# Optimization experiments

Hardware: AMD Instinct MI355X
Metric: run time of the kernel (lower is better)

The kernel has to match this reference:

```python
import jax, jax.numpy as jnp
import numpy as np

N_NODES = 50000
N_EDGES = 800000
N_GRAPHS = 50
N_OBS = 4
N_FEAT = 64
N_LAYERS = 3


def setup_inputs() -> dict:
    key = jax.random.key(0)
    ks = jax.random.split(key, 12)
    x = jax.random.normal(ks[0], (N_NODES, N_OBS), dtype=jnp.float32)
    # every node appears at least once as a target (col) so degree > 0 everywhere
    row = jax.random.randint(ks[1], (N_EDGES,), 0, N_NODES, dtype=jnp.int32)
    col = jnp.concatenate([
        jnp.arange(N_NODES, dtype=jnp.int32),
        jax.random.randint(ks[2], (N_EDGES - N_NODES,), 0, N_NODES, dtype=jnp.int32),
    ])
    edge_index = jnp.stack([row, col])  # [2, E]
    batch = jnp.repeat(jnp.arange(N_GRAPHS, dtype=jnp.int32), N_NODES // N_GRAPHS)

    def w(k, shape):
        fan_in = shape[0]
        return jax.random.normal(k, shape, dtype=jnp.float32) / jnp.sqrt(jnp.float32(fan_in))

    return {
        "x": x,
        "W_init": w(ks[3], (N_OBS, N_FEAT)),
        "W_e1": w(ks[4], (N_OBS, N_FEAT - 1)),
        "W_e2": w(ks[5], (N_FEAT, N_FEAT)),
        "W_msg": w(ks[6], (N_LAYERS, 2 * N_FEAT, N_FEAT)),
        "W_upd": w(ks[7], (N_LAYERS, 2 * N_FEAT, N_FEAT)),
        "W_pool": w(ks[8], (N_FEAT, N_FEAT)),
        "W_read": w(ks[9], (2 * N_FEAT, 1)),
        "b_read": jnp.zeros((1,), dtype=jnp.float32),
        "edge_index": edge_index,
        "batch": batch,
        "batch_size": N_GRAPHS,
    }


def reference(x, W_init, W_e1, W_e2, W_msg, W_upd, W_pool, W_read, b_read,
              edge_index, batch, batch_size):
    n = x.shape[0]
    row, col = edge_index[0], edge_index[1]
    # in-degree at target nodes (PyG degree(col, N))
    deg = jax.ops.segment_sum(jnp.ones_like(col, dtype=x.dtype), col, num_segments=n)
    deg_inv = (1.0 / deg)[:, None]  # [N,1]

    # node init embedding
    cur = jax.nn.relu(x @ W_init)  # [N,F]

    # EdgeAndNodeEmbeddingLayer
    h = jax.nn.relu(x @ W_e1)  # [N,F-1]
    agg = deg_inv * jax.ops.segment_sum(h[row], col, num_segments=n)  # [N,F-1]
    y = jnp.concatenate([agg, (deg / deg.max())[:, None]], axis=1)  # [N,F]
    edge_emb = jax.nn.relu(y @ W_e2)  # [N,F]

    # UpdateNodeEmbeddingLayer x n_layers
    for i in range(W_msg.shape[0]):
        nagg = deg_inv * jax.ops.segment_sum(cur[row], col, num_segments=n)
        msg = jax.nn.relu(jnp.concatenate([nagg, edge_emb], axis=-1) @ W_msg[i])
        cur = jax.nn.relu(jnp.concatenate([cur, msg], axis=-1) @ W_upd[i])

    # ReadoutLayer (graphs are equal-sized, batch is sorted -> means[batch])
    counts = jax.ops.segment_sum(jnp.ones((n,), dtype=x.dtype), batch, num_segments=batch_size)
    means = jax.ops.segment_sum(cur, batch, num_segments=batch_size) / counts[:, None]
    global_pool = means[batch]  # [N,F]
    f_pooled = global_pool @ W_pool
    features = jax.nn.relu(jnp.concatenate([f_pooled, cur], axis=-1))  # [N,2F]
    out = features @ W_read + b_read  # [N,1]
    return out
```

## Files before the change

### kernel.cpp

```cpp
#include <hip/hip_runtime.h>
#include <hip/hip_bf16.h>

#define N_NODES 50000
#define N_EDGES 800000
#define NF      64
#define NG      50
#define NPG     (N_NODES / NG)
#define SCAN_NBLK ((N_NODES + 255) / 256)
#define MCHUNK  20
#define MROWS   (NPG / MCHUNK)
#define NTILES  (N_NODES / 16)
#define GATHER_BLKS ((NTILES + 3) / 4)
#define FP_CHUNKS 896
#define FP_CHSZ  ((N_EDGES + FP_CHUNKS - 1) / FP_CHUNKS)
#define FP_NPP   (N_NODES / 8)
#define DEG_BLKS (FP_CHUNKS * 8)
#define INIT_BLKS ((N_NODES * 32 + 255) / 256)
#define DEGS 5

typedef __attribute__((ext_vector_type(8))) short bf16x8;
typedef __attribute__((ext_vector_type(4))) float f32x4;
typedef unsigned short u16;
typedef unsigned char u8;

__device__ inline unsigned pkbf(float a, float b) {
    unsigned ua = __float_as_uint(a) + 0x8000u;
    unsigned ub = __float_as_uint(b) + 0x8000u;
    return (ua >> 16) | (ub & 0xFFFF0000u);
}
__device__ inline short bf1(float a) {
    return (short)((__float_as_uint(a) + 0x8000u) >> 16);
}
__device__ inline float lo2f(unsigned u) { return __uint_as_float(u << 16); }
__device__ inline float hi2f(unsigned u) { return __uint_as_float(u & 0xFFFF0000u); }
__device__ inline void accp(float2* a, uint4 v) {
    a[0].x += lo2f(v.x); a[0].y += hi2f(v.x);
    a[1].x += lo2f(v.y); a[1].y += hi2f(v.y);
    a[2].x += lo2f(v.z); a[2].y += hi2f(v.z);
    a[3].x += lo2f(v.w); a[3].y += hi2f(v.w);
}

__global__ void k_deg_init(const int* __restrict__ col, int* __restrict__ deg,
                           u8* __restrict__ epos,
                           const float* __restrict__ x, const float* __restrict__ Wi,
                           const float* __restrict__ We1,
                           u16* __restrict__ cur, u16* __restrict__ h) {
    if (blockIdx.x < DEG_BLKS) {
        int part = blockIdx.x & 7, chunk = blockIdx.x >> 3;
        int lo = part * FP_NPP, hi = lo + FP_NPP;
        int e0 = chunk * FP_CHSZ;
        int e1 = min(N_EDGES, e0 + FP_CHSZ);
        for (int e = e0 + threadIdx.x; e < e1; e += 256) {
            int c = col[e];
            if (c >= lo && c < hi) {
                int pos = atomicAdd(&deg[c << DEGS], 1);
                epos[e] = (u8)pos;
            }
        }
        return;
    }
    int idx = (blockIdx.x - DEG_BLKS) * 256 + threadIdx.x;
    int node = idx >> 5, q = idx & 31;
    if (node >= N_NODES) return;
    int f0 = 2 * q, f1 = 2 * q + 1;
    float4 xv = ((const float4*)x)[node];
    float c0 = xv.x * Wi[f0] + xv.y * Wi[64 + f0] + xv.z * Wi[128 + f0] + xv.w * Wi[192 + f0];
    float c1 = xv.x * Wi[f1] + xv.y * Wi[64 + f1] + xv.z * Wi[128 + f1] + xv.w * Wi[192 + f1];
    ((unsigned*)cur)[node * 32 + q] = pkbf(fmaxf(c0, 0.f), fmaxf(c1, 0.f));
    float h0 = xv.x * We1[f0] + xv.y * We1[63 + f0] + xv.z * We1[126 + f0] + xv.w * We1[189 + f0];
    h0 = fmaxf(h0, 0.f);
    float h1 = 0.f;
    if (f1 < 63) {
        h1 = xv.x * We1[f1] + xv.y * We1[63 + f1] + xv.z * We1[126 + f1] + xv.w * We1[189 + f1];
        h1 = fmaxf(h1, 0.f);
    }
    ((unsigned*)h)[node * 32 + q] = pkbf(h0, h1);
}

__global__ void k_blocksum(const int* __restrict__ deg, int* __restrict__ partials,
                           int* __restrict__ dmax, int* __restrict__ hist) {
    __shared__ int lh[256];
    int t = threadIdx.x;
    lh[t] = 0;
    __syncthreads();
    int i = blockIdx.x * 256 + t;
    int d = (i < N_NODES) ? deg[i << DEGS] : 0;
    if (i < N_NODES) atomicAdd(&lh[min(d, 255)], 1);
    int v = d, m = d;
    for (int off = 32; off; off >>= 1) {
        v += __shfl_xor(v, off, 64);
        m = max(m, __shfl_xor(m, off, 64));
    }
    __shared__ int s[4];
    if ((t & 63) == 0) { s[t >> 6] = v; atomicMax(dmax, m); }
    __syncthreads();
    if (t == 0) partials[blockIdx.x] = s[0] + s[1] + s[2] + s[3];
    if (lh[t]) atomicAdd(&hist[t], lh[t]);
}

__global__ __launch_bounds__(256) void k_scanfinal2(
        const int* __restrict__ deg, const int* __restrict__ partials,
        const int* __restrict__ hist, int* __restrict__ rowptr,
        int* __restrict__ binBump, int* __restrict__ perm) {
    int b = blockIdx.x, t = threadIdx.x;
    __shared__ int lh[256], lbase[256];
    lh[t] = 0;
    int p = (t < b) ? partials[t] : 0;
    for (int off = 32; off; off >>= 1) p += __shfl_xor(p, off, 64);
    __shared__ int sr[4];
    if ((t & 63) == 0) sr[t >> 6] = p;
    __syncthreads();
    int prev = sr[0] + sr[1] + sr[2] + sr[3];
    int i = b * 256 + t;
    int v = (i < N_NODES) ? deg[i << DEGS] : 0;
    int bin = min(v, 255);
    int rank = 0;
    if (i < N_NODES) rank = atomicAdd(&lh[bin], 1);
    __shared__ int s[256];
    int hv = hist[t];
    s[t] = hv;
    __syncthreads();
    for (int off = 1; off < 256; off <<= 1) {
        int u = (t >= off) ? s[t - off] : 0;
        __syncthreads();
        s[t] += u;
        __syncthreads();
    }
    int hpref = s[t] - hv;
    __syncthreads();
    s[t] = v;
    __syncthreads();
    for (int off = 1; off < 256; off <<= 1) {
        int u = (t >= off) ? s[t - off] : 0;
        __syncthreads();
        s[t] += u;
        __syncthreads();
    }
    int ex = prev + s[t] - v;
    if (i < N_NODES) rowptr[i] = ex;
    if (b == 0 && t == 0) rowptr[N_NODES] = N_EDGES;
    __syncthreads();
    if (lh[t] > 0) lbase[t] = hpref + atomicAdd(&binBump[t], lh[t]);
    __syncthreads();
    if (i < N_NODES) perm[lbase[bin] + rank] = i;
}

__global__ void k_fill(const int* __restrict__ row, const int* __restrict__ col,
                       const int* __restrict__ rowptr, const u8* __restrict__ epos,
                       u16* __restrict__ csr) {
    int part = blockIdx.x & 7, chunk = blockIdx.x >> 3;
    int lo = part * FP_NPP, hi = lo + FP_NPP;
    int e0 = chunk * FP_CHSZ;
    int e1 = min(N_EDGES, e0 + FP_CHSZ);
    for (int e = e0 + threadIdx.x; e < e1; e += 256) {
        int c = col[e];
        if (c >= lo && c < hi)
            csr[rowptr[c] + epos[e]] = (u16)row[e];
    }
}

__device__ inline void gather_tile(const u16* __restrict__ src,
                                   const int* __restrict__ rowptr,
                                   const u16* __restrict__ csr,
                                   int node, int m, int q, int wv,
                                   short (*AT)[16][64]) {
    int beg = rowptr[node], end = rowptr[node + 1];
    float2 ac[8];
#pragma unroll
    for (int i = 0; i < 8; i++) ac[i] = make_float2(0.f, 0.f);
    int j = beg;
    for (; j + 3 < end; j += 4) {
        int r0 = csr[j], r1 = csr[j + 1], r2 = csr[j + 2], r3 = csr[j + 3];
        const uint4* p0 = (const uint4*)(src + (size_t)r0 * 64 + q * 16);
        const uint4* p1 = (const uint4*)(src + (size_t)r1 * 64 + q * 16);
        const uint4* p2 = (const uint4*)(src + (size_t)r2 * 64 + q * 16);
        const uint4* p3 = (const uint4*)(src + (size_t)r3 * 64 + q * 16);
        uint4 v00 = p0[0], v01 = p0[1];
        uint4 v10 = p1[0], v11 = p1[1];
        uint4 v20 = p2[0], v21 = p2[1];
        uint4 v30 = p3[0], v31 = p3[1];
        accp(ac, v00); accp(ac + 4, v01);
        accp(ac, v10); accp(ac + 4, v11);
        accp(ac, v20); accp(ac + 4, v21);
        accp(ac, v30); accp(ac + 4, v31);
    }
    for (; j < end; j++) {
        int r = csr[j];
        const uint4* p = (const uint4*)(src + (size_t)r * 64 + q * 16);
        uint4 v0 = p[0], v1 = p[1];
        accp(ac, v0); accp(ac + 4, v1);
    }
    float inv = 1.0f / (float)(end - beg);
    uint4 lo, hi;
    lo.x = pkbf(ac[0].x * inv, ac[0].y * inv);
    lo.y = pkbf(ac[1].x * inv, ac[1].y * inv);
    lo.z = pkbf(ac[2].x * inv, ac[2].y * inv);
    lo.w = pkbf(ac[3].x * inv, ac[3].y * inv);
    hi.x = pkbf(ac[4].x * inv, ac[4].y * inv);
    hi.y = pkbf(ac[5].x * inv, ac[5].y * inv);
    hi.z = pkbf(ac[6].x * inv, ac[6].y * inv);
    hi.w = pkbf(ac[7].x * inv, ac[7].y * inv);
    *(uint4*)&AT[wv][m][((2 * q) ^ (m & 7)) * 8]     = lo;
    *(uint4*)&AT[wv][m][((2 * q + 1) ^ (m & 7)) * 8] = hi;
}

__global__ __launch_bounds__(256) void k_edge_f(
        const u16* __restrict__ h, const int* __restrict__ rowptr,
        const u16* __restrict__ csr, const int* __restrict__ dmax,
        const float* __restrict__ We2, const int* __restrict__ perm,
        u16* __restrict__ ee) {
    __shared__ unsigned SB[2][4][64][4];
    __shared__ short AT[4][16][64];
    int t = threadIdx.x;
    for (int F = t; F < 512; F += 256) {
        int ks = F >> 8, tile = (F >> 6) & 3, ln = F & 63;
        int c = ln & 15, qq = ln >> 4;
        const float* W = We2 + (ks * 32 + qq * 8) * 64 + tile * 16 + c;
        unsigned d0 = pkbf(W[0],       W[64]);
        unsigned d1 = pkbf(W[2 * 64],  W[3 * 64]);
        unsigned d2 = pkbf(W[4 * 64],  W[5 * 64]);
        unsigned d3 = pkbf(W[6 * 64],  W[7 * 64]);
        int slot = ln ^ ((ln >> 3) & 7);
        SB[ks][tile][slot][0] = d0; SB[ks][tile][slot][1] = d1;
        SB[ks][tile][slot][2] = d2; SB[ks][tile][slot][3] = d3;
    }
    __syncthreads();
    int wv = t >> 6, lane = t & 63;
    int m = lane & 15, quad = lane >> 4;
    int slot = lane ^ ((lane >> 3) & 7);
    float idm = 1.0f / (float)dmax[0];
    for (int tb = blockIdx.x * 4 + wv; tb < NTILES; tb += gridDim.x * 4) {
        int base = tb * 16;
        int pn = perm[base + m];
        gather_tile(h, rowptr, csr, pn, m, quad, wv, AT);
        float dv = (float)(rowptr[pn + 1] - rowptr[pn]) * idm;
        int prw[4];
#pragma unroll
        for (int r = 0; r < 4; r++) prw[r] = perm[base + quad * 4 + r];
        f32x4 acc[4];
#pragma unroll
        for (int i = 0; i < 4; i++) acc[i] = (f32x4){0.f, 0.f, 0.f, 0.f};
#pragma unroll
        for (int ks = 0; ks < 2; ks++) {
            int gp = (ks * 4 + quad) ^ (m & 7);
            bf16x8 a = *(const bf16x8*)&AT[wv][m][gp * 8];
            if (ks == 1 && quad == 3) a[7] = bf1(dv);
#pragma unroll
            for (int tile = 0; tile < 4; tile++) {
                bf16x8 b = *(const bf16x8*)&SB[ks][tile][slot][0];
                acc[tile] = __builtin_amdgcn_mfma_f32_16x16x32_bf16(a, b, acc[tile], 0, 0, 0);
            }
        }
#pragma unroll
        for (int tile = 0; tile < 4; tile++)
#pragma unroll
            for (int r = 0; r < 4; r++)
                ee[(size_t)prw[r] * 64 + tile * 16 + m] =
                    (u16)bf1(fmaxf(acc[tile][r], 0.f));
    }
}

template <bool F32OUT>
__global__ __launch_bounds__(256) void k_flayer(
        const u16* __restrict__ cur, const u16* __restrict__ ee,
        const int* __restrict__ rowptr, const u16* __restrict__ csr,
        const float* __restrict__ Wm, const float* __restrict__ Wu,
        const int* __restrict__ perm, void* __restrict__ outp) {
    __shared__ unsigned SB[2][4][4][64][4];
    __shared__ short XT[4][16][64];
    int t = threadIdx.x;
    for (int F = t; F < 2048; F += 256) {
        int g = F >> 10, ks = (F >> 8) & 3, tile = (F >> 6) & 3, ln = F & 63;
        int c = ln & 15, qq = ln >> 4;
        const float* W = (g ? Wu : Wm) + (ks * 32 + qq * 8) * 64 + tile * 16 + c;
        unsigned d0 = pkbf(W[0],      W[64]);
        unsigned d1 = pkbf(W[2 * 64], W[3 * 64]);
        unsigned d2 = pkbf(W[4 * 64], W[5 * 64]);
        unsigned d3 = pkbf(W[6 * 64], W[7 * 64]);
        int slot = ln ^ ((ln >> 3) & 7);
        SB[g][ks][tile][slot][0] = d0; SB[g][ks][tile][slot][1] = d1;
        SB[g][ks][tile][slot][2] = d2; SB[g][ks][tile][slot][3] = d3;
    }
    __syncthreads();
    int wv = t >> 6, lane = t & 63;
    int m = lane & 15, quad = lane >> 4;
    int slot = lane ^ ((lane >> 3) & 7);
    for (int tb = blockIdx.x * 4 + wv; tb < NTILES; tb += gridDim.x * 4) {
        int base = tb * 16;
        int pn = perm[base + m];
        gather_tile(cur, rowptr, csr, pn, m, quad, wv, XT);
        const u16* erow = ee  + (size_t)pn * 64;
        const u16* crow = cur + (size_t)pn * 64;
        int prw[4];
#pragma unroll
        for (int r = 0; r < 4; r++) prw[r] = perm[base + quad * 4 + r];
        f32x4 acc[4];
#pragma unroll
        for (int i = 0; i < 4; i++) acc[i] = (f32x4){0.f, 0.f, 0.f, 0.f};
#pragma unroll
        for (int ks = 0; ks < 4; ks++) {
            bf16x8 a;
            if (ks < 2) {
                int gp = (ks * 4 + quad) ^ (m & 7);
                a = *(const bf16x8*)&XT[wv][m][gp * 8];
            } else {
                a = *(const bf16x8*)(erow + (ks - 2) * 32 + quad * 8);
            }
#pragma unroll
            for (int tile = 0; tile < 4; tile++) {
                bf16x8 b = *(const bf16x8*)&SB[0][ks][tile][slot][0];
                acc[tile] = __builtin_amdgcn_mfma_f32_16x16x32_bf16(a, b, acc[tile], 0, 0, 0);
            }
        }
#pragma unroll
        for (int tile = 0; tile < 4; tile++)
#pragma unroll
            for (int r = 0; r < 4; r++) {
                int node = quad * 4 + r;
                int f = tile * 16 + m;
                int sidx = (((f >> 3) ^ (node & 7)) << 3) | (f & 7);
                XT[wv][node][sidx] = bf1(fmaxf(acc[tile][r], 0.f));
            }
#pragma unroll
        for (int i = 0; i < 4; i++) acc[i] = (f32x4){0.f, 0.f, 0.f, 0.f};
#pragma unroll
        for (int ks = 0; ks < 4; ks++) {
            bf16x8 a;
            if (ks < 2) {
                a = *(const bf16x8*)(crow + ks * 32 + quad * 8);
            } else {
                int gp = ((ks - 2) * 4 + quad) ^ (m & 7);
                a = *(const bf16x8*)&XT[wv][m][gp << 3];
            }
#pragma unroll
            for (int tile = 0; tile < 4; tile++) {
                bf16x8 b = *(const bf16x8*)&SB[1][ks][tile][slot][0];
                acc[tile] = __builtin_amdgcn_mfma_f32_16x16x32_bf16(a, b, acc[tile], 0, 0, 0);
            }
        }
#pragma unroll
        for (int tile = 0; tile < 4; tile++)
#pragma unroll
            for (int r = 0; r < 4; r++) {
                float v = fmaxf(acc[tile][r], 0.f);
                size_t oi = (size_t)prw[r] * 64 + tile * 16 + m;
                if (F32OUT) ((float*)outp)[oi] = v;
                else        ((u16*)outp)[oi] = (u16)bf1(v);
            }
    }
}

__global__ __launch_bounds__(256) void k_means2(const float* __restrict__ cur,
                                                float* __restrict__ pmeans) {
    int g = blockIdx.x / MCHUNK;
    int c = blockIdx.x % MCHUNK;
    int t = threadIdx.x, f = t & 63, q = t >> 6;
    int base = g * NPG + c * MROWS;
    float acc = 0.f;
    for (int n = base + q; n < base + MROWS; n += 4) acc += cur[(size_t)n * 64 + f];
    __shared__ float red[4][64];
    red[q][f] = acc;
    __syncthreads();
    if (q == 0)
        pmeans[(size_t)(g * MCHUNK + c) * 64 + f] =
            red[0][f] + red[1][f] + red[2][f] + red[3][f];
}

__global__ __launch_bounds__(256) void k_pool2(
        const float* __restrict__ pmeans, const float* __restrict__ Wp,
        const float* __restrict__ Wr, float* __restrict__ r1) {
    __shared__ float sm[4][64];
    int wv = threadIdx.x >> 6, lane = threadIdx.x & 63;
    for (int g = wv; g < NG; g += 4) {
        float m = 0.f;
        const float* pm = pmeans + (size_t)g * MCHUNK * 64 + lane;
#pragma unroll
        for (int c = 0; c < MCHUNK; c++) m += pm[c * 64];
        sm[wv][lane] = m * (1.0f / NPG);
        float a2 = 0.f;
#pragma unroll 16
        for (int k = 0; k < 64; k++) a2 = fmaf(sm[wv][k], Wp[k * 64 + lane], a2);
        float v = fmaxf(a2, 0.f) * Wr[lane];
        for (int off = 32; off; off >>= 1) v += __shfl_xor(v, off, 64);
        if (lane == 0) r1[g] = v;
    }
}

__global__ void k_read2(const float* __restrict__ cur, const float* __restrict__ r1,
                        const int* __restrict__ batch, const float* __restrict__ Wr,
                        const float* __restrict__ br, float* __restrict__ out) {
    int idx = blockIdx.x * 256 + threadIdx.x;
    int node = idx >> 4;
    if (node >= N_NODES) return;
    int q = idx & 15;
    float4 c = *(const float4*)(cur + (size_t)node * 64 + q * 4);
    float4 w = *(const float4*)(Wr + 64 + q * 4);
    float v = fmaxf(c.x, 0.f) * w.x + fmaxf(c.y, 0.f) * w.y
            + fmaxf(c.z, 0.f) * w.z + fmaxf(c.w, 0.f) * w.w;
    v += __shfl_xor(v, 1, 64); v += __shfl_xor(v, 2, 64);
    v += __shfl_xor(v, 4, 64); v += __shfl_xor(v, 8, 64);
    if (q == 0) out[node] = v + r1[batch[node]] + br[0];
}

extern "C" void kernel_launch(void* const* d_in, const int* in_sizes, int n_in,
                              void* d_out, int out_size, void* d_ws, size_t ws_size,
                              hipStream_t stream) {
    const float* x    = (const float*)d_in[0];
    const float* Wi   = (const float*)d_in[1];
    const float* We1  = (const float*)d_in[2];
    const float* We2  = (const float*)d_in[3];
    const float* Wm   = (const float*)d_in[4];
    const float* Wu   = (const float*)d_in[5];
    const float* Wp   = (const float*)d_in[6];
    const float* Wr   = (const float*)d_in[7];
    const float* br   = (const float*)d_in[8];
    const int*   ei   = (const int*)d_in[9];
    const int*   batch= (const int*)d_in[10];
    const int* row = ei;
    const int* col = ei + N_EDGES;
    float* out = (float*)d_out;

    char* w = (char*)d_ws;
    size_t off = 0;
    auto carve = [&](size_t bytes) -> void* {
        void* p = (void*)(w + off);
        off += (bytes + 255) & ~(size_t)255;
        return p;
    };
    int*   deg      = (int*)carve((size_t)N_NODES * 4 * 32);
    int*   dmax     = (int*)carve(256);
    int*   hist     = (int*)carve(256 * 4);
    int*   binBump  = (int*)carve(256 * 4);
    size_t zero_span = off;
    int*   rowptr   = (int*)carve((size_t)(N_NODES + 1) * 4);
    u8*    epos     = (u8*)carve((size_t)N_EDGES);
    u16*   csr      = (u16*)carve((size_t)N_EDGES * 2);
    int*   partials = (int*)carve((size_t)SCAN_NBLK * 4);
    int*   perm     = (int*)carve((size_t)N_NODES * 4);
    float* pmeans   = (float*)carve((size_t)NG * MCHUNK * 64 * 4);
    u16*   bufA     = (u16*)carve((size_t)N_NODES * 64 * 2);
    u16*   bufB     = (u16*)carve((size_t)N_NODES * 64 * 2);
    u16*   ee       = (u16*)carve((size_t)N_NODES * 64 * 2);
    float* curF     = (float*)carve((size_t)N_NODES * 64 * 4);
    float* r1       = (float*)carve((size_t)NG * 4);

    hipMemsetAsync(d_ws, 0, zero_span, stream);

    k_deg_init<<<DEG_BLKS + INIT_BLKS, 256, 0, stream>>>(col, deg, epos,
                                                         x, Wi, We1, bufA, bufB);
    k_blocksum  <<<SCAN_NBLK, 256, 0, stream>>>(deg, partials, dmax, hist);
    k_scanfinal2<<<SCAN_NBLK, 256, 0, stream>>>(deg, partials, hist, rowptr,
                                                binBump, perm);
    k_fill      <<<DEG_BLKS, 256, 0, stream>>>(row, col, rowptr, epos, csr);

    k_edge_f<<<GATHER_BLKS, 256, 0, stream>>>(bufB, rowptr, csr, dmax, We2, perm, ee);

    k_flayer<false><<<GATHER_BLKS, 256, 0, stream>>>(bufA, ee, rowptr, csr,
                                                     Wm, Wu, perm, bufB);
    k_flayer<false><<<GATHER_BLKS, 256, 0, stream>>>(bufB, ee, rowptr, csr,
                                                     Wm + 128 * 64, Wu + 128 * 64, perm, bufA);
    k_flayer<true> <<<GATHER_BLKS, 256, 0, stream>>>(bufA, ee, rowptr, csr,
                                                     Wm + 2 * 128 * 64, Wu + 2 * 128 * 64,
                                                     perm, curF);

    k_means2<<<NG * MCHUNK, 256, 0, stream>>>(curF, pmeans);
    k_pool2 <<<1, 256, 0, stream>>>(pmeans, Wp, Wr, r1);
    k_read2<<<(N_NODES * 16 + 255) / 256, 256, 0, stream>>>(curF, r1, batch, Wr, br, out);
}
```

Before: 307.8 us.

## Split fused gather+MFMA kernels into separate gather and dense-transform kernels

Moves the neighbor mean-aggregation out of the edge-embedding and layer kernels into a standalone gather kernel that writes a bf16 aggregate buffer. The dense kernels then read the aggregate row directly from global memory instead of from LDS. This is meant to let the latency-bound gather run without the LDS and register footprint of the MFMA kernels, which could raise occupancy. In exchange it adds four kernel launches and an extra 6.4 MB write and read of the aggregate per layer.

After: 318.8 us. 1.04x slower.

```diff
diff --git a/kernel.cpp b/kernel.cpp
--- a/kernel.cpp
+++ b/kernel.cpp
@@ -159,58 +159,61 @@
     }
 }
 
-__device__ inline void gather_tile(const u16* __restrict__ src,
-                                   const int* __restrict__ rowptr,
-                                   const u16* __restrict__ csr,
-                                   int node, int m, int q, int wv,
-                                   short (*AT)[16][64]) {
-    int beg = rowptr[node], end = rowptr[node + 1];
-    float2 ac[8];
-#pragma unroll
-    for (int i = 0; i < 8; i++) ac[i] = make_float2(0.f, 0.f);
-    int j = beg;
-    for (; j + 3 < end; j += 4) {
-        int r0 = csr[j], r1 = csr[j + 1], r2 = csr[j + 2], r3 = csr[j + 3];
-        const uint4* p0 = (const uint4*)(src + (size_t)r0 * 64 + q * 16);
-        const uint4* p1 = (const uint4*)(src + (size_t)r1 * 64 + q * 16);
-        const uint4* p2 = (const uint4*)(src + (size_t)r2 * 64 + q * 16);
-        const uint4* p3 = (const uint4*)(src + (size_t)r3 * 64 + q * 16);
-        uint4 v00 = p0[0], v01 = p0[1];
-        uint4 v10 = p1[0], v11 = p1[1];
-        uint4 v20 = p2[0], v21 = p2[1];
-        uint4 v30 = p3[0], v31 = p3[1];
-        accp(ac, v00); accp(ac + 4, v01);
-        accp(ac, v10); accp(ac + 4, v11);
-        accp(ac, v20); accp(ac + 4, v21);
-        accp(ac, v30); accp(ac + 4, v31);
-    }
-    for (; j < end; j++) {
-        int r = csr[j];
-        const uint4* p = (const uint4*)(src + (size_t)r * 64 + q * 16);
-        uint4 v0 = p[0], v1 = p[1];
-        accp(ac, v0); accp(ac + 4, v1);
-    }
-    float inv = 1.0f / (float)(end - beg);
-    uint4 lo, hi;
-    lo.x = pkbf(ac[0].x * inv, ac[0].y * inv);
-    lo.y = pkbf(ac[1].x * inv, ac[1].y * inv);
-    lo.z = pkbf(ac[2].x * inv, ac[2].y * inv);
-    lo.w = pkbf(ac[3].x * inv, ac[3].y * inv);
-    hi.x = pkbf(ac[4].x * inv, ac[4].y * inv);
-    hi.y = pkbf(ac[5].x * inv, ac[5].y * inv);
-    hi.z = pkbf(ac[6].x * inv, ac[6].y * inv);
-    hi.w = pkbf(ac[7].x * inv, ac[7].y * inv);
-    *(uint4*)&AT[wv][m][((2 * q) ^ (m & 7)) * 8]     = lo;
-    *(uint4*)&AT[wv][m][((2 * q + 1) ^ (m & 7)) * 8] = hi;
-}
-
-__global__ __launch_bounds__(256) void k_edge_f(
-        const u16* __restrict__ h, const int* __restrict__ rowptr,
-        const u16* __restrict__ csr, const int* __restrict__ dmax,
-        const float* __restrict__ We2, const int* __restrict__ perm,
-        u16* __restrict__ ee) {
+__global__ __launch_bounds__(256) void k_gather(
+        const u16* __restrict__ src, const int* __restrict__ rowptr,
+        const u16* __restrict__ csr, const int* __restrict__ perm,
+        u16* __restrict__ agg) {
+    int t = threadIdx.x, wv = t >> 6, lane = t & 63;
+    int m = lane & 15, q = lane >> 4;
+    for (int tb = blockIdx.x * 4 + wv; tb < NTILES; tb += gridDim.x * 4) {
+        int pn = perm[tb * 16 + m];
+        int beg = rowptr[pn], end = rowptr[pn + 1];
+        float2 ac[8];
+#pragma unroll
+        for (int i = 0; i < 8; i++) ac[i] = make_float2(0.f, 0.f);
+        int j = beg;
+        for (; j + 3 < end; j += 4) {
+            int r0 = csr[j], r1 = csr[j + 1], r2 = csr[j + 2], r3 = csr[j + 3];
+            const uint4* p0 = (const uint4*)(src + (size_t)r0 * 64 + q * 16);
+            const uint4* p1 = (const uint4*)(src + (size_t)r1 * 64 + q * 16);
+            const uint4* p2 = (const uint4*)(src + (size_t)r2 * 64 + q * 16);
+            const uint4* p3 = (const uint4*)(src + (size_t)r3 * 64 + q * 16);
+            uint4 v00 = p0[0], v01 = p0[1];
+            uint4 v10 = p1[0], v11 = p1[1];
+            uint4 v20 = p2[0], v21 = p2[1];
+            uint4 v30 = p3[0], v31 = p3[1];
+            accp(ac, v00); accp(ac + 4, v01);
+            accp(ac, v10); accp(ac + 4, v11);
+            accp(ac, v20); accp(ac + 4, v21);
+            accp(ac, v30); accp(ac + 4, v31);
+        }
+        for (; j < end; j++) {
+            int r = csr[j];
+            const uint4* p = (const uint4*)(src + (size_t)r * 64 + q * 16);
+            uint4 v0 = p[0], v1 = p[1];
+            accp(ac, v0); accp(ac + 4, v1);
+        }
+        float inv = 1.0f / (float)(end - beg);
+        uint4 lo, hi;
+        lo.x = pkbf(ac[0].x * inv, ac[0].y * inv);
+        lo.y = pkbf(ac[1].x * inv, ac[1].y * inv);
+        lo.z = pkbf(ac[2].x * inv, ac[2].y * inv);
+        lo.w = pkbf(ac[3].x * inv, ac[3].y * inv);
+        hi.x = pkbf(ac[4].x * inv, ac[4].y * inv);
+        hi.y = pkbf(ac[5].x * inv, ac[5].y * inv);
+        hi.z = pkbf(ac[6].x * inv, ac[6].y * inv);
+        hi.w = pkbf(ac[7].x * inv, ac[7].y * inv);
+        u16* arow = agg + (size_t)pn * 64 + q * 16;
+        *(uint4*)arow       = lo;
+        *(uint4*)(arow + 8) = hi;
+    }
+}
+
+__global__ __launch_bounds__(256) void k_edge2(
+        const u16* __restrict__ agg, const int* __restrict__ rowptr,
+        const int* __restrict__ dmax, const float* __restrict__ We2,
+        const int* __restrict__ perm, u16* __restrict__ ee) {
     __shared__ unsigned SB[2][4][64][4];
-    __shared__ short AT[4][16][64];
     int t = threadIdx.x;
     for (int F = t; F < 512; F += 256) {
         int ks = F >> 8, tile = (F >> 6) & 3, ln = F & 63;
@@ -232,7 +235,7 @@
     for (int tb = blockIdx.x * 4 + wv; tb < NTILES; tb += gridDim.x * 4) {
         int base = tb * 16;
         int pn = perm[base + m];
-        gather_tile(h, rowptr, csr, pn, m, quad, wv, AT);
+        const u16* arow = agg + (size_t)pn * 64;
         float dv = (float)(rowptr[pn + 1] - rowptr[pn]) * idm;
         int prw[4];
 #pragma unroll
@@ -242,8 +245,7 @@
         for (int i = 0; i < 4; i++) acc[i] = (f32x4){0.f, 0.f, 0.f, 0.f};
 #pragma unroll
         for (int ks = 0; ks < 2; ks++) {
-            int gp = (ks * 4 + quad) ^ (m & 7);
-            bf16x8 a = *(const bf16x8*)&AT[wv][m][gp * 8];
+            bf16x8 a = *(const bf16x8*)(arow + ks * 32 + quad * 8);
             if (ks == 1 && quad == 3) a[7] = bf1(dv);
 #pragma unroll
             for (int tile = 0; tile < 4; tile++) {
@@ -261,9 +263,9 @@
 }
 
 template <bool F32OUT>
-__global__ __launch_bounds__(256) void k_flayer(
-        const u16* __restrict__ cur, const u16* __restrict__ ee,
-        const int* __restrict__ rowptr, const u16* __restrict__ csr,
+__global__ __launch_bounds__(256) void k_layer2(
+        const u16* __restrict__ agg, const u16* __restrict__ ee,
+        const u16* __restrict__ cur,
         const float* __restrict__ Wm, const float* __restrict__ Wu,
         const int* __restrict__ perm, void* __restrict__ outp) {
     __shared__ unsigned SB[2][4][4][64][4];
@@ -288,7 +290,7 @@
     for (int tb = blockIdx.x * 4 + wv; tb < NTILES; tb += gridDim.x * 4) {
         int base = tb * 16;
         int pn = perm[base + m];
-        gather_tile(cur, rowptr, csr, pn, m, quad, wv, XT);
+        const u16* arow = agg + (size_t)pn * 64;
         const u16* erow = ee  + (size_t)pn * 64;
         const u16* crow = cur + (size_t)pn * 64;
         int prw[4];
@@ -299,13 +301,9 @@
         for (int i = 0; i < 4; i++) acc[i] = (f32x4){0.f, 0.f, 0.f, 0.f};
 #pragma unroll
         for (int ks = 0; ks < 4; ks++) {
-            bf16x8 a;
-            if (ks < 2) {
-                int gp = (ks * 4 + quad) ^ (m & 7);
-                a = *(const bf16x8*)&XT[wv][m][gp * 8];
-            } else {
-                a = *(const bf16x8*)(erow + (ks - 2) * 32 + quad * 8);
-            }
+            bf16x8 a = (ks < 2)
+                ? *(const bf16x8*)(arow + ks * 32 + quad * 8)
+                : *(const bf16x8*)(erow + (ks - 2) * 32 + quad * 8);
 #pragma unroll
             for (int tile = 0; tile < 4; tile++) {
                 bf16x8 b = *(const bf16x8*)&SB[0][ks][tile][slot][0];
@@ -438,6 +436,7 @@
     int*   partials = (int*)carve((size_t)SCAN_NBLK * 4);
     int*   perm     = (int*)carve((size_t)N_NODES * 4);
     float* pmeans   = (float*)carve((size_t)NG * MCHUNK * 64 * 4);
+    u16*   agg      = (u16*)carve((size_t)N_NODES * 64 * 2);
     u16*   bufA     = (u16*)carve((size_t)N_NODES * 64 * 2);
     u16*   bufB     = (u16*)carve((size_t)N_NODES * 64 * 2);
     u16*   ee       = (u16*)carve((size_t)N_NODES * 64 * 2);
@@ -453,13 +452,17 @@
                                                 binBump, perm);
     k_fill      <<<DEG_BLKS, 256, 0, stream>>>(row, col, rowptr, epos, csr);
 
-    k_edge_f<<<GATHER_BLKS, 256, 0, stream>>>(bufB, rowptr, csr, dmax, We2, perm, ee);
-
-    k_flayer<false><<<GATHER_BLKS, 256, 0, stream>>>(bufA, ee, rowptr, csr,
-                                                     Wm, Wu, perm, bufB);
-    k_flayer<false><<<GATHER_BLKS, 256, 0, stream>>>(bufB, ee, rowptr, csr,
-                                                     Wm + 128 * 64, Wu + 128 * 64, perm, bufA);
-    k_flayer<true> <<<GATHER_BLKS, 256, 0, stream>>>(bufA, ee, rowptr, csr,
+    k_gather<<<GATHER_BLKS, 256, 0, stream>>>(bufB, rowptr, csr, perm, agg);
+    k_edge2 <<<GATHER_BLKS, 256, 0, stream>>>(agg, rowptr, dmax, We2, perm, ee);
+
+    k_gather<<<GATHER_BLKS, 256, 0, stream>>>(bufA, rowptr, csr, perm, agg);
+    k_layer2<false><<<GATHER_BLKS, 256, 0, stream>>>(agg, ee, bufA, Wm, Wu, perm, bufB);
+    k_gather<<<GATHER_BLKS, 256, 0, stream>>>(bufB, rowptr, csr, perm, agg);
+    k_layer2<false><<<GATHER_BLKS, 256, 0, stream>>>(agg, ee, bufB,
+                                                     Wm + 128 * 64, Wu + 128 * 64,
+                                                     perm, bufA);
+    k_gather<<<GATHER_BLKS, 256, 0, stream>>>(bufA, rowptr, csr, perm, agg);
+    k_layer2<true> <<<GATHER_BLKS, 256, 0, stream>>>(agg, ee, bufA,
                                                      Wm + 2 * 128 * 64, Wu + 2 * 128 * 64,
                                                      perm, curF);
 
```
